# Kernel tuning notes

Measured on AMD Instinct MI355X. Metric: run time of the kernel, lower is better.

## Reference

```python
import jax, jax.numpy as jnp
import numpy as np

LN_EPS = 1e-5


def _forward(x, conv_w, conv_b, ln_w, ln_b, in_proj_w, in_proj_b, out_proj_w, out_proj_b):
    # x: (1, duration, dimensions)
    B, Dur, Dim = x.shape
    xt = jnp.transpose(x, (0, 2, 1))  # (1, Dim, Dur) -> Conv1d NCH layout
    branches = []
    for b in range(Dur):  # structural loop over the 32 conv branches (kernel size k=b+1)
        k = b + 1
        L = Dur - b  # output length duration - k + 1
        w = conv_w[b, :, :, :k]  # (Dim_out, Dim_in, k); padded taps beyond k unused
        y = jax.lax.conv_general_dilated(
            xt, w, window_strides=(1,), padding='VALID',
            dimension_numbers=('NCH', 'OIH', 'NCH'))  # (1, Dim, L)
        y = y + conv_b[b][None, :, None]
        y = jax.nn.gelu(y, approximate=False)  # torch nn.GELU default is exact erf form
        # LayerNorm(normalized_shape=[1, Dim, L]) with batch==1 normalizes the whole tensor
        mu = jnp.mean(y)
        var = jnp.var(y)  # biased, matching torch LayerNorm
        y = (y - mu) * jax.lax.rsqrt(var + LN_EPS)
        y = y * ln_w[b, :, :L][None] + ln_b[b, :, :L][None]
        branches.append(y)  # dropout is identity at inference (p=0.0)
    xc = jnp.concatenate(branches, axis=2)  # (1, Dim, T), T = Dur*(Dur+1)//2
    T = xc.shape[2]

    # nn.MultiheadAttention(embed_dim=T, num_heads=T), batch_first=False: input (L=1, N=Dim, E=T).
    # With seq_len==1, softmax over the single key is exactly 1, so attention output is
    # out_proj(v_proj(value)). value_i = x[:, i, :] broadcast over N, so every batch row of
    # output_i equals out_proj(v_proj(xc[0, i])). Summing over i (the feature loop):
    Wv = in_proj_w[2 * T:]          # (T, T) value slice of in_proj
    bv = in_proj_b[2 * T:]          # (T,)
    V = xc[0] @ Wv.T + bv           # (Dim, T): row i is v-proj of feature i
    S = V.sum(axis=0) @ out_proj_w.T + Dim * out_proj_b  # (T,)  sum over the Dim-term loop
    xa = jnp.broadcast_to(S[None, None, :], (1, Dim, T))  # identical rows, as in torch

    # x.unfold(2, Dur, 4*Dur).mean(-1)
    step = 4 * Dur
    n_w = (T - Dur) // step + 1
    idx = jnp.arange(n_w)[:, None] * step + jnp.arange(Dur)[None, :]  # (n_w, Dur)
    pooled = xa[:, :, idx].mean(-1)  # (1, Dim, n_w)
    return jnp.transpose(pooled, (0, 2, 1))  # (1, n_w, Dim)


def setup_inputs() -> dict:
    key = jax.random.key(0)
    ks = jax.random.split(key, 6)
    Dur, Dim = 32, 256
    T = Dur * (Dur + 1) // 2  # 528
    x = jax.random.normal(ks[0], (1, Dur, Dim), jnp.float32)
    conv_w = jax.random.normal(ks[1], (Dur, Dim, Dim, Dur), jnp.float32) * 0.02  # padded kernel bank
    conv_b = jax.random.normal(ks[2], (Dur, Dim), jnp.float32) * 0.02
    ln_w = jnp.ones((Dur, Dim, Dur), jnp.float32)   # branch b uses [:, :, :Dur-b]
    ln_b = jnp.zeros((Dur, Dim, Dur), jnp.float32)
    in_proj_w = jax.random.normal(ks[3], (3 * T, T), jnp.float32) * 0.02
    in_proj_b = jnp.zeros((3 * T,), jnp.float32)
    out_proj_w = jax.random.normal(ks[4], (T, T), jnp.float32) * 0.02
    out_proj_b = jnp.zeros((T,), jnp.float32)
    return {"x": x, "conv_w": conv_w, "conv_b": conv_b, "ln_w": ln_w, "ln_b": ln_b,
            "in_proj_w": in_proj_w, "in_proj_b": in_proj_b,
            "out_proj_w": out_proj_w, "out_proj_b": out_proj_b}


def reference(x, conv_w, conv_b, ln_w, ln_b, in_proj_w, in_proj_b, out_proj_w, out_proj_b):
    return _forward(x, conv_w, conv_b, ln_w, ln_b, in_proj_w, in_proj_b, out_proj_w, out_proj_b)
```

## Files before the change

kernel.cpp:

```cpp
#include <hip/hip_runtime.h>
#include <math.h>

#define DUR 32
#define DIM 256
#define TT  528

#define WS_BSUM 0
#define WS_BSQ  32
#define WS_CY   64
#define WS_CW   592
#define WS_CB   1120
#define WS_S    1648
#define WS_ZERO_FLOATS 592

__device__ __forceinline__ float gelu_exact(float v) {
    return 0.5f * v * (1.0f + erff(v * 0.70710678118654752f));
}

__device__ __forceinline__ float wave_reduce_down(float v) {
    v += __shfl_down(v, 32, 64);
    v += __shfl_down(v, 16, 64);
    v += __shfl_down(v, 8, 64);
    v += __shfl_down(v, 4, 64);
    v += __shfl_down(v, 2, 64);
    v += __shfl_down(v, 1, 64);
    return v;
}

template<int BB>
__device__ __forceinline__ void wave_body(
    const int o, const int lane,
    const float* __restrict__ x, const float* __restrict__ W,
    const float* __restrict__ convb, const float* __restrict__ lnw,
    float* __restrict__ ws)
{
    constexpr int k  = BB + 1;
    constexpr int L  = DUR - BB;
    constexpr int K4 = (k + 3) / 4;

    const float* Wo = W + (size_t)(BB * DIM + o) * (DIM * DUR);

    float4 wbuf[2][K4];
    {
        const float* Wl = Wo + (size_t)lane * DUR;
#pragma unroll
        for (int m = 0; m < K4; ++m) wbuf[0][m] = *(const float4*)(Wl + 4 * m);
    }

    float acc[L];
#pragma unroll
    for (int t = 0; t < L; ++t) acc[t] = 0.f;

#pragma unroll
    for (int c = 0; c < 4; ++c) {
        const int cur = c & 1, nxt = cur ^ 1;
        if (c < 3) {
            const float* Wl = Wo + (size_t)((c + 1) * 64 + lane) * DUR;
#pragma unroll
            for (int m = 0; m < K4; ++m) wbuf[nxt][m] = *(const float4*)(Wl + 4 * m);
        }
        const int i = c * 64 + lane;
        float xv[32];
#pragma unroll
        for (int tau = 0; tau < 32; ++tau) xv[tau] = x[tau * DIM + i];
#pragma unroll
        for (int tau = 0; tau < 32; ++tau) asm volatile("" : "+v"(xv[tau]));
#pragma unroll
        for (int m = 0; m < K4; ++m) {
            asm volatile("" : "+v"(wbuf[cur][m].x), "+v"(wbuf[cur][m].y),
                              "+v"(wbuf[cur][m].z), "+v"(wbuf[cur][m].w));
        }
#pragma unroll
        for (int t = 0; t < L; ++t) {
#pragma unroll
            for (int m = 0; m < K4; ++m) {
                acc[t] = fmaf(xv[t + 4*m + 0], wbuf[cur][m].x, acc[t]);
                if (4*m + 1 < k) acc[t] = fmaf(xv[t + 4*m + 1], wbuf[cur][m].y, acc[t]);
                if (4*m + 2 < k) acc[t] = fmaf(xv[t + 4*m + 2], wbuf[cur][m].z, acc[t]);
                if (4*m + 3 < k) acc[t] = fmaf(xv[t + 4*m + 3], wbuf[cur][m].w, acc[t]);
            }
        }
    }

    float mine = 0.f;
#pragma unroll
    for (int t = 0; t < L; ++t) {
        float v = acc[t];
        v += __shfl_xor(v, 1, 64);
        v += __shfl_xor(v, 2, 64);
        v += __shfl_xor(v, 4, 64);
        v += __shfl_xor(v, 8, 64);
        v += __shfl_xor(v, 16, 64);
        v += __shfl_xor(v, 32, 64);
        if (lane == t) mine = v;
    }

    constexpr int tg = BB * DUR - (BB * (BB - 1)) / 2;
    float g = 0.f;
    if (lane < L) {
        const float y = mine + convb[BB * DIM + o];
        g = gelu_exact(y);
        const float lw = lnw[((size_t)(BB * DIM + o)) * DUR + lane];
        atomicAdd(ws + WS_CY + tg + lane, g * lw);
    }
    const float s1 = wave_reduce_down(g);
    const float s2 = wave_reduce_down(g * g);
    if (lane == 0) {
        atomicAdd(ws + WS_BSUM + BB, s1);
        atomicAdd(ws + WS_BSQ  + BB, s2);
    }
}

__global__ __launch_bounds__(256, 4) void conv_kernel(
    const float* __restrict__ x, const float* __restrict__ W,
    const float* __restrict__ convb, const float* __restrict__ lnw,
    const float* __restrict__ lnb, float* __restrict__ ws)
{
    const int bid = blockIdx.x;
    const int n = threadIdx.x;
    if (bid >= 2048) {
        const int pb = bid - 2048;
        int b = 0, off = 0;
        while (pb >= off + (DUR - b)) { off += DUR - b; ++b; }
        const int t = pb - off;
        const float lw = lnw[((size_t)(b * DIM + n)) * DUR + t];
        const float lb = lnb[((size_t)(b * DIM + n)) * DUR + t];
        __shared__ float rw[4], rb[4];
        const int wave = n >> 6, lane = n & 63;
        const float a = wave_reduce_down(lw);
        const float c = wave_reduce_down(lb);
        if (lane == 0) { rw[wave] = a; rb[wave] = c; }
        __syncthreads();
        if (n == 0) {
            ws[WS_CW + pb] = rw[0] + rw[1] + rw[2] + rw[3];
            ws[WS_CB + pb] = rb[0] + rb[1] + rb[2] + rb[3];
        }
        return;
    }

    const int bb   = (13 * ((bid & 31) + (bid >> 8))) & 31;
    const int o    = (bid >> 5) * 4 + (n >> 6);
    const int lane = n & 63;
    switch (bb) {
        case  0: wave_body< 0>(o, lane, x, W, convb, lnw, ws); break;
        case  1: wave_body< 1>(o, lane, x, W, convb, lnw, ws); break;
        case  2: wave_body< 2>(o, lane, x, W, convb, lnw, ws); break;
        case  3: wave_body< 3>(o, lane, x, W, convb, lnw, ws); break;
        case  4: wave_body< 4>(o, lane, x, W, convb, lnw, ws); break;
        case  5: wave_body< 5>(o, lane, x, W, convb, lnw, ws); break;
        case  6: wave_body< 6>(o, lane, x, W, convb, lnw, ws); break;
        case  7: wave_body< 7>(o, lane, x, W, convb, lnw, ws); break;
        case  8: wave_body< 8>(o, lane, x, W, convb, lnw, ws); break;
        case  9: wave_body< 9>(o, lane, x, W, convb, lnw, ws); break;
        case 10: wave_body<10>(o, lane, x, W, convb, lnw, ws); break;
        case 11: wave_body<11>(o, lane, x, W, convb, lnw, ws); break;
        case 12: wave_body<12>(o, lane, x, W, convb, lnw, ws); break;
        case 13: wave_body<13>(o, lane, x, W, convb, lnw, ws); break;
        case 14: wave_body<14>(o, lane, x, W, convb, lnw, ws); break;
        case 15: wave_body<15>(o, lane, x, W, convb, lnw, ws); break;
        case 16: wave_body<16>(o, lane, x, W, convb, lnw, ws); break;
        case 17: wave_body<17>(o, lane, x, W, convb, lnw, ws); break;
        case 18: wave_body<18>(o, lane, x, W, convb, lnw, ws); break;
        case 19: wave_body<19>(o, lane, x, W, convb, lnw, ws); break;
        case 20: wave_body<20>(o, lane, x, W, convb, lnw, ws); break;
        case 21: wave_body<21>(o, lane, x, W, convb, lnw, ws); break;
        case 22: wave_body<22>(o, lane, x, W, convb, lnw, ws); break;
        case 23: wave_body<23>(o, lane, x, W, convb, lnw, ws); break;
        case 24: wave_body<24>(o, lane, x, W, convb, lnw, ws); break;
        case 25: wave_body<25>(o, lane, x, W, convb, lnw, ws); break;
        case 26: wave_body<26>(o, lane, x, W, convb, lnw, ws); break;
        case 27: wave_body<27>(o, lane, x, W, convb, lnw, ws); break;
        case 28: wave_body<28>(o, lane, x, W, convb, lnw, ws); break;
        case 29: wave_body<29>(o, lane, x, W, convb, lnw, ws); break;
        case 30: wave_body<30>(o, lane, x, W, convb, lnw, ws); break;
        default: wave_body<31>(o, lane, x, W, convb, lnw, ws); break;
    }
}

__global__ __launch_bounds__(256) void proj1_kernel(
    float* ws, const float* __restrict__ in_proj_w,
    const float* __restrict__ in_proj_b)
{
    __shared__ float cc[TT];
    __shared__ float mu_s[32], r_s[32];
    __shared__ int map[TT];
    const int n = threadIdx.x;
    if (n < 32) {
        const int Lb = 32 - n;
        const float cnt = 256.f * (float)Lb;
        const float mu = ws[WS_BSUM + n] / cnt;
        const float var = ws[WS_BSQ + n] / cnt - mu * mu;
        mu_s[n] = mu;
        r_s[n] = rsqrtf(var + 1e-5f);
        const int off = n * 32 - (n * (n - 1)) / 2;
        for (int t = 0; t < Lb; ++t) map[off + t] = n;
    }
    __syncthreads();
    for (int t = n; t < TT; t += 256) {
        const int b = map[t];
        cc[t] = (ws[WS_CY + t] - mu_s[b] * ws[WS_CW + t]) * r_s[b] + ws[WS_CB + t];
    }
    __syncthreads();
    const int wave = n >> 6, lane = n & 63;
    const int row = blockIdx.x * 4 + wave;
    const float* Wr = in_proj_w + (size_t)(2 * TT + row) * TT;
    float a = 0.f;
    for (int t = lane; t < TT; t += 64) a = fmaf(Wr[t], cc[t], a);
    a = wave_reduce_down(a);
    if (lane == 0) ws[WS_S + row] = a + 256.f * in_proj_b[2 * TT + row];
}

__global__ __launch_bounds__(256) void proj2_kernel(
    const float* __restrict__ ws, const float* __restrict__ out_proj_w,
    const float* __restrict__ out_proj_b, float* __restrict__ out)
{
    const int w = blockIdx.x, n = threadIdx.x;
    const int wave = n >> 6, lane = n & 63;
    __shared__ float s2s[32];
    __shared__ float mv;
    for (int jj = 0; jj < 8; ++jj) {
        const int j = wave * 8 + jj;
        const int u = w * 128 + j;
        const float* Or = out_proj_w + (size_t)u * TT;
        float a = 0.f;
        for (int t = lane; t < TT; t += 64) a = fmaf(Or[t], ws[WS_S + t], a);
        a = wave_reduce_down(a);
        if (lane == 0) s2s[j] = a + 256.f * out_proj_b[u];
    }
    __syncthreads();
    if (n < 64) {
        float v = (n < 32) ? s2s[n] : 0.f;
        v += __shfl_down(v, 16, 64);
        v += __shfl_down(v, 8, 64);
        v += __shfl_down(v, 4, 64);
        v += __shfl_down(v, 2, 64);
        v += __shfl_down(v, 1, 64);
        if (n == 0) mv = v * (1.0f / 32.0f);
    }
    __syncthreads();
    out[w * 256 + n] = mv;
}

extern "C" void kernel_launch(void* const* d_in, const int* in_sizes, int n_in,
                              void* d_out, int out_size, void* d_ws, size_t ws_size,
                              hipStream_t stream)
{
    const float* x   = (const float*)d_in[0];
    const float* W   = (const float*)d_in[1];
    const float* cb  = (const float*)d_in[2];
    const float* lnw = (const float*)d_in[3];
    const float* lnb = (const float*)d_in[4];
    const float* ipw = (const float*)d_in[5];
    const float* ipb = (const float*)d_in[6];
    const float* opw = (const float*)d_in[7];
    const float* opb = (const float*)d_in[8];
    float* ws  = (float*)d_ws;
    float* out = (float*)d_out;

    hipMemsetAsync(ws, 0, WS_ZERO_FLOATS * sizeof(float), stream);
    conv_kernel<<<2048 + TT, 256, 0, stream>>>(x, W, cb, lnw, lnb, ws);
    proj1_kernel<<<132, 256, 0, stream>>>(ws, ipw, ipb);
    proj2_kernel<<<4, 256, 0, stream>>>(ws, opw, opb, out);
}
```

Measured before the change: 451.8 us.

## Pair short and long conv branches per block and template on tap groups

Result: slower. 506.9 us (+12.2%).

```diff
diff --git a/kernel.cpp b/kernel.cpp
--- a/kernel.cpp
+++ b/kernel.cpp
@@ -27,87 +27,91 @@
     return v;
 }
 
-template<int BB>
+template<int K4>
 __device__ __forceinline__ void wave_body(
-    const int o, const int lane,
+    const int bb, const int o, const int lane,
     const float* __restrict__ x, const float* __restrict__ W,
     const float* __restrict__ convb, const float* __restrict__ lnw,
     float* __restrict__ ws)
 {
-    constexpr int k  = BB + 1;
-    constexpr int L  = DUR - BB;
-    constexpr int K4 = (k + 3) / 4;
-
-    const float* Wo = W + (size_t)(BB * DIM + o) * (DIM * DUR);
-
-    float4 wbuf[2][K4];
+    const int k = bb + 1;
+    const int L = DUR - bb;
+    constexpr int MAXL = (36 - 4 * K4) > 32 ? 32 : (36 - 4 * K4);
+
+    const float* Wo = W + (size_t)(bb * DIM + o) * (DIM * DUR);
+
+    float4 wb[2][K4];
     {
         const float* Wl = Wo + (size_t)lane * DUR;
 #pragma unroll
-        for (int m = 0; m < K4; ++m) wbuf[0][m] = *(const float4*)(Wl + 4 * m);
-    }
-
-    float acc[L];
-#pragma unroll
-    for (int t = 0; t < L; ++t) acc[t] = 0.f;
-
-#pragma unroll
+        for (int m = 0; m < K4; ++m) wb[0][m] = *(const float4*)(Wl + 4 * m);
+    }
+
+    float acc[MAXL];
+#pragma unroll
+    for (int t = 0; t < MAXL; ++t) acc[t] = 0.f;
+
+#pragma unroll 1
     for (int c = 0; c < 4; ++c) {
-        const int cur = c & 1, nxt = cur ^ 1;
+        const int cur = c & 1;
         if (c < 3) {
             const float* Wl = Wo + (size_t)((c + 1) * 64 + lane) * DUR;
 #pragma unroll
-            for (int m = 0; m < K4; ++m) wbuf[nxt][m] = *(const float4*)(Wl + 4 * m);
+            for (int m = 0; m < K4; ++m) wb[cur ^ 1][m] = *(const float4*)(Wl + 4 * m);
         }
         const int i = c * 64 + lane;
-        float xv[32];
+        float xv[35];
 #pragma unroll
         for (int tau = 0; tau < 32; ++tau) xv[tau] = x[tau * DIM + i];
-#pragma unroll
-        for (int tau = 0; tau < 32; ++tau) asm volatile("" : "+v"(xv[tau]));
+        xv[32] = 0.f; xv[33] = 0.f; xv[34] = 0.f;
 #pragma unroll
         for (int m = 0; m < K4; ++m) {
-            asm volatile("" : "+v"(wbuf[cur][m].x), "+v"(wbuf[cur][m].y),
-                              "+v"(wbuf[cur][m].z), "+v"(wbuf[cur][m].w));
-        }
-#pragma unroll
-        for (int t = 0; t < L; ++t) {
-#pragma unroll
-            for (int m = 0; m < K4; ++m) {
-                acc[t] = fmaf(xv[t + 4*m + 0], wbuf[cur][m].x, acc[t]);
-                if (4*m + 1 < k) acc[t] = fmaf(xv[t + 4*m + 1], wbuf[cur][m].y, acc[t]);
-                if (4*m + 2 < k) acc[t] = fmaf(xv[t + 4*m + 2], wbuf[cur][m].z, acc[t]);
-                if (4*m + 3 < k) acc[t] = fmaf(xv[t + 4*m + 3], wbuf[cur][m].w, acc[t]);
+            if (4 * m + 1 >= k) wb[cur][m].y = 0.f;
+            if (4 * m + 2 >= k) wb[cur][m].z = 0.f;
+            if (4 * m + 3 >= k) wb[cur][m].w = 0.f;
+        }
+#pragma unroll
+        for (int t = 0; t < MAXL; ++t) {
+            if (t < L) {
+#pragma unroll
+                for (int m = 0; m < K4; ++m) {
+                    acc[t] = fmaf(xv[t + 4*m + 0], wb[cur][m].x, acc[t]);
+                    acc[t] = fmaf(xv[t + 4*m + 1], wb[cur][m].y, acc[t]);
+                    acc[t] = fmaf(xv[t + 4*m + 2], wb[cur][m].z, acc[t]);
+                    acc[t] = fmaf(xv[t + 4*m + 3], wb[cur][m].w, acc[t]);
+                }
             }
         }
     }
 
     float mine = 0.f;
 #pragma unroll
-    for (int t = 0; t < L; ++t) {
-        float v = acc[t];
-        v += __shfl_xor(v, 1, 64);
-        v += __shfl_xor(v, 2, 64);
-        v += __shfl_xor(v, 4, 64);
-        v += __shfl_xor(v, 8, 64);
-        v += __shfl_xor(v, 16, 64);
-        v += __shfl_xor(v, 32, 64);
-        if (lane == t) mine = v;
-    }
-
-    constexpr int tg = BB * DUR - (BB * (BB - 1)) / 2;
+    for (int t = 0; t < MAXL; ++t) {
+        if (t < L) {
+            float v = acc[t];
+            v += __shfl_xor(v, 1, 64);
+            v += __shfl_xor(v, 2, 64);
+            v += __shfl_xor(v, 4, 64);
+            v += __shfl_xor(v, 8, 64);
+            v += __shfl_xor(v, 16, 64);
+            v += __shfl_xor(v, 32, 64);
+            if (lane == t) mine = v;
+        }
+    }
+
+    const int tg = bb * DUR - (bb * (bb - 1)) / 2;
     float g = 0.f;
     if (lane < L) {
-        const float y = mine + convb[BB * DIM + o];
+        const float y = mine + convb[bb * DIM + o];
         g = gelu_exact(y);
-        const float lw = lnw[((size_t)(BB * DIM + o)) * DUR + lane];
+        const float lw = lnw[((size_t)(bb * DIM + o)) * DUR + lane];
         atomicAdd(ws + WS_CY + tg + lane, g * lw);
     }
     const float s1 = wave_reduce_down(g);
     const float s2 = wave_reduce_down(g * g);
     if (lane == 0) {
-        atomicAdd(ws + WS_BSUM + BB, s1);
-        atomicAdd(ws + WS_BSQ  + BB, s2);
+        atomicAdd(ws + WS_BSUM + bb, s1);
+        atomicAdd(ws + WS_BSQ  + bb, s2);
     }
 }
 
@@ -138,42 +142,21 @@
         return;
     }
 
-    const int bb   = (13 * ((bid & 31) + (bid >> 8))) & 31;
-    const int o    = (bid >> 5) * 4 + (n >> 6);
+    const int p    = bid & 15;
+    const int og   = bid >> 4;
+    const int w    = n >> 6;
     const int lane = n & 63;
-    switch (bb) {
-        case  0: wave_body< 0>(o, lane, x, W, convb, lnw, ws); break;
-        case  1: wave_body< 1>(o, lane, x, W, convb, lnw, ws); break;
-        case  2: wave_body< 2>(o, lane, x, W, convb, lnw, ws); break;
-        case  3: wave_body< 3>(o, lane, x, W, convb, lnw, ws); break;
-        case  4: wave_body< 4>(o, lane, x, W, convb, lnw, ws); break;
-        case  5: wave_body< 5>(o, lane, x, W, convb, lnw, ws); break;
-        case  6: wave_body< 6>(o, lane, x, W, convb, lnw, ws); break;
-        case  7: wave_body< 7>(o, lane, x, W, convb, lnw, ws); break;
-        case  8: wave_body< 8>(o, lane, x, W, convb, lnw, ws); break;
-        case  9: wave_body< 9>(o, lane, x, W, convb, lnw, ws); break;
-        case 10: wave_body<10>(o, lane, x, W, convb, lnw, ws); break;
-        case 11: wave_body<11>(o, lane, x, W, convb, lnw, ws); break;
-        case 12: wave_body<12>(o, lane, x, W, convb, lnw, ws); break;
-        case 13: wave_body<13>(o, lane, x, W, convb, lnw, ws); break;
-        case 14: wave_body<14>(o, lane, x, W, convb, lnw, ws); break;
-        case 15: wave_body<15>(o, lane, x, W, convb, lnw, ws); break;
-        case 16: wave_body<16>(o, lane, x, W, convb, lnw, ws); break;
-        case 17: wave_body<17>(o, lane, x, W, convb, lnw, ws); break;
-        case 18: wave_body<18>(o, lane, x, W, convb, lnw, ws); break;
-        case 19: wave_body<19>(o, lane, x, W, convb, lnw, ws); break;
-        case 20: wave_body<20>(o, lane, x, W, convb, lnw, ws); break;
-        case 21: wave_body<21>(o, lane, x, W, convb, lnw, ws); break;
-        case 22: wave_body<22>(o, lane, x, W, convb, lnw, ws); break;
-        case 23: wave_body<23>(o, lane, x, W, convb, lnw, ws); break;
-        case 24: wave_body<24>(o, lane, x, W, convb, lnw, ws); break;
-        case 25: wave_body<25>(o, lane, x, W, convb, lnw, ws); break;
-        case 26: wave_body<26>(o, lane, x, W, convb, lnw, ws); break;
-        case 27: wave_body<27>(o, lane, x, W, convb, lnw, ws); break;
-        case 28: wave_body<28>(o, lane, x, W, convb, lnw, ws); break;
-        case 29: wave_body<29>(o, lane, x, W, convb, lnw, ws); break;
-        case 30: wave_body<30>(o, lane, x, W, convb, lnw, ws); break;
-        default: wave_body<31>(o, lane, x, W, convb, lnw, ws); break;
+    const int bb   = (w < 2) ? p : 31 - p;
+    const int o    = og * 2 + (w & 1);
+    switch (bb >> 2) {
+        case 0:  wave_body<1>(bb, o, lane, x, W, convb, lnw, ws); break;
+        case 1:  wave_body<2>(bb, o, lane, x, W, convb, lnw, ws); break;
+        case 2:  wave_body<3>(bb, o, lane, x, W, convb, lnw, ws); break;
+        case 3:  wave_body<4>(bb, o, lane, x, W, convb, lnw, ws); break;
+        case 4:  wave_body<5>(bb, o, lane, x, W, convb, lnw, ws); break;
+        case 5:  wave_body<6>(bb, o, lane, x, W, convb, lnw, ws); break;
+        case 6:  wave_body<7>(bb, o, lane, x, W, convb, lnw, ws); break;
+        default: wave_body<8>(bb, o, lane, x, W, convb, lnw, ws); break;
     }
 }
 
```
